# Kernel tuning notes

Measured on AMD Instinct MI355X. Metric: run time of the kernel, lower is better.

Reference implementation:

```python
import jax, jax.numpy as jnp
import numpy as np

B, HIST = 1024, 50
USER_NUM, ITEM_NUM, IN_CH = 100000, 100000, 64

def setup_inputs() -> dict:
    key = jax.random.key(0)
    k1, k2, k3, k4 = jax.random.split(key, 4)
    # xavier_uniform bound = sqrt(6/(fan_in+fan_out))
    bu = np.sqrt(6.0 / (USER_NUM + IN_CH))
    bi = np.sqrt(6.0 / (ITEM_NUM + IN_CH))
    return {
        "user_emb": jax.random.uniform(k1, (USER_NUM, IN_CH), jnp.float32, -bu, bu),
        "item_emb": jax.random.uniform(k2, (ITEM_NUM, IN_CH), jnp.float32, -bi, bi),
        "center_uid": jax.random.randint(k3, (B,), 0, USER_NUM, jnp.int32),
        "seq": jax.random.randint(k4, (B, HIST), 0, ITEM_NUM, jnp.int32),
    }

def reference(user_emb, item_emb, center_uid, seq):
    # gather selected users: [B, C]
    sel = user_emb[center_uid]
    # dense preference scores: [B, item_num]
    pref_score = sel @ item_emb.T
    b, n_items = pref_score.shape
    # boolean positive mask built by scattering seq indices per row
    rows = jnp.arange(b)[:, None]                      # [B,1]
    mask = jnp.zeros((b, n_items), bool).at[rows, seq].set(True)
    # loss = sum (s-1)^2 over positives + sum s^2 over negatives
    loss = jnp.sum(jnp.where(mask, (pref_score - 1.0) ** 2, pref_score ** 2))
    return loss, pref_score
```

## Files before the change

### kernel.cpp

```cpp
#include <hip/hip_runtime.h>

#define M_DIM 1024
#define N_DIM 100000
#define K_DIM 64
#define HIST 50

#define BM 64
#define BN 128
#define BMP 68
#define BNP 132

#define SEL_OFF 0
#define ITEM_OFF (K_DIM * BMP)
#define LDS_FLOATS (K_DIM * BMP + K_DIM * BNP)

__global__ __launch_bounds__(256, 3) void gemm_loss_kernel(
    const float* __restrict__ user_emb, const float* __restrict__ item_emb,
    const int* __restrict__ center_uid, float* __restrict__ out)
{
    __shared__ __align__(16) float lds[LDS_FLOATS];
    __shared__ float red[4];
    const int tid = threadIdx.x;
    const int bm0 = blockIdx.x * BM;
    const int bi0 = blockIdx.y * BN;

    {
        const int k4 = tid & 15;
        const int r0 = tid >> 4;
        #pragma unroll
        for (int it = 0; it < 4; ++it) {
            const int r = r0 + 16 * it;
            const int uid = center_uid[bm0 + r];
            const float4 v = *reinterpret_cast<const float4*>(
                user_emb + (size_t)uid * K_DIM + k4 * 4);
            float* p = &lds[SEL_OFF + (k4 * 4) * BMP + r];
            p[0 * BMP] = v.x; p[1 * BMP] = v.y; p[2 * BMP] = v.z; p[3 * BMP] = v.w;
        }
    }
    {
        const int k4 = tid & 15;
        const int i0 = tid >> 4;
        #pragma unroll
        for (int it = 0; it < 8; ++it) {
            const int i = i0 + 16 * it;
            const int gi = bi0 + i;
            float4 v = make_float4(0.f, 0.f, 0.f, 0.f);
            if (gi < N_DIM)
                v = *reinterpret_cast<const float4*>(
                    item_emb + (size_t)gi * K_DIM + k4 * 4);
            float* p = &lds[ITEM_OFF + (k4 * 4) * BNP + i];
            p[0 * BNP] = v.x; p[1 * BNP] = v.y; p[2 * BNP] = v.z; p[3 * BNP] = v.w;
        }
    }
    __syncthreads();

    const int tx = tid & 31;
    const int ty = tid >> 5;

    float acc[8][4];
    #pragma unroll
    for (int r = 0; r < 8; ++r)
        #pragma unroll
        for (int c = 0; c < 4; ++c) acc[r][c] = 0.f;

    const float* aBase = &lds[SEL_OFF + ty * 8];
    const float* bBase = &lds[ITEM_OFF + tx];

    #pragma unroll 8
    for (int k = 0; k < K_DIM; ++k) {
        const float4 a01 = *reinterpret_cast<const float4*>(aBase + k * BMP);
        const float4 a23 = *reinterpret_cast<const float4*>(aBase + k * BMP + 4);
        float b[4];
        #pragma unroll
        for (int c = 0; c < 4; ++c) b[c] = bBase[k * BNP + 32 * c];
        const float a[8] = {a01.x, a01.y, a01.z, a01.w, a23.x, a23.y, a23.z, a23.w};
        #pragma unroll
        for (int r = 0; r < 8; ++r)
            #pragma unroll
            for (int c = 0; c < 4; ++c)
                acc[r][c] = fmaf(a[r], b[c], acc[r][c]);
    }

    float ss = 0.f;
    float* pref = out + 1;
    #pragma unroll
    for (int r = 0; r < 8; ++r) {
        const size_t row = (size_t)(bm0 + ty * 8 + r) * N_DIM;
        #pragma unroll
        for (int c = 0; c < 4; ++c) {
            const int col = bi0 + tx + 32 * c;
            if (col < N_DIM) {
                const float v = acc[r][c];
                pref[row + col] = v;
                ss = fmaf(v, v, ss);
            }
        }
    }
    #pragma unroll
    for (int off = 32; off > 0; off >>= 1) ss += __shfl_xor(ss, off, 64);
    if ((tid & 63) == 0) red[tid >> 6] = ss;
    __syncthreads();
    if (tid == 0)
        atomicAdd(out, red[0] + red[1] + red[2] + red[3]);
}

__global__ __launch_bounds__(64) void pos_kernel(
    const float* __restrict__ user_emb, const float* __restrict__ item_emb,
    const int* __restrict__ center_uid, const int* __restrict__ seq,
    float* __restrict__ out)
{
    const int b = blockIdx.x;
    const int lane = threadIdx.x;
    const int sv = (lane < HIST) ? seq[b * HIST + lane] : -1;
    const int uid = center_uid[b];
    const float selv = user_emb[(size_t)uid * K_DIM + lane];
    float corr = 0.f;
    for (int h = 0; h < HIST; ++h) {
        const int i = __shfl(sv, h, 64);
        const unsigned long long dup = __ballot(lane < h && sv == i);
        if (dup == 0ull) {
            float p = selv * item_emb[(size_t)i * K_DIM + lane];
            #pragma unroll
            for (int off = 32; off > 0; off >>= 1) p += __shfl_xor(p, off, 64);
            if (lane == 0) corr += 1.f - 2.f * p;
        }
    }
    if (lane == 0) atomicAdd(out, corr);
}

extern "C" void kernel_launch(void* const* d_in, const int* in_sizes, int n_in,
                              void* d_out, int out_size, void* d_ws, size_t ws_size,
                              hipStream_t stream) {
    const float* user_emb  = (const float*)d_in[0];
    const float* item_emb  = (const float*)d_in[1];
    const int*   center_uid = (const int*)d_in[2];
    const int*   seq        = (const int*)d_in[3];
    float* out = (float*)d_out;

    hipMemsetAsync(out, 0, sizeof(float), stream);
    pos_kernel<<<dim3(M_DIM), dim3(64), 0, stream>>>(
        user_emb, item_emb, center_uid, seq, out);
    dim3 grid(M_DIM / BM, (N_DIM + BN - 1) / BN);
    gemm_loss_kernel<<<grid, dim3(256), 0, stream>>>(
        user_emb, item_emb, center_uid, out);
}
```

Before: 664.5 us.

## Use split-bf16 MFMA GEMM with swizzled LDS and XCD-aware tile remap

```diff
diff --git a/kernel.cpp b/kernel.cpp
--- a/kernel.cpp
+++ b/kernel.cpp
@@ -7,98 +7,148 @@
 
 #define BM 64
 #define BN 128
-#define BMP 68
-#define BNP 132
+#define NBLK_M (M_DIM / BM)
+#define NBLK_N ((N_DIM + BN - 1) / BN)
+#define NWG (NBLK_M * NBLK_N)
+#define WG_PER_XCD (NWG / 8)
 
-#define SEL_OFF 0
-#define ITEM_OFF (K_DIM * BMP)
-#define LDS_FLOATS (K_DIM * BMP + K_DIM * BNP)
+typedef __attribute__((ext_vector_type(8))) short bfrag_t;
+typedef __attribute__((ext_vector_type(16))) float accv_t;
 
-__global__ __launch_bounds__(256, 3) void gemm_loss_kernel(
+__device__ __forceinline__ unsigned short f2bf(float f) {
+    const unsigned u = __float_as_uint(f);
+    return (unsigned short)((u + 0x7FFFu + ((u >> 16) & 1u)) >> 16);
+}
+
+__global__ __launch_bounds__(256, 4) void gemm_loss_kernel(
     const float* __restrict__ user_emb, const float* __restrict__ item_emb,
     const int* __restrict__ center_uid, float* __restrict__ out)
 {
-    __shared__ __align__(16) float lds[LDS_FLOATS];
+    __shared__ __align__(16) unsigned char ldsHi[BN * 128];
+    __shared__ __align__(16) unsigned char ldsLo[BN * 128];
     __shared__ float red[4];
+
     const int tid = threadIdx.x;
-    const int bm0 = blockIdx.x * BM;
-    const int bi0 = blockIdx.y * BN;
+
+    const int bid   = blockIdx.x;
+    const int idx   = (bid & 7) * WG_PER_XCD + (bid >> 3);
+    const int itile = idx >> 4;
+    const int mtile = idx & 15;
+    const int bm0 = mtile * BM;
+    const int bi0 = itile * BN;
 
     {
-        const int k4 = tid & 15;
-        const int r0 = tid >> 4;
+        const int r  = tid >> 1;
+        const int h  = tid & 1;
+        const int gi = bi0 + r;
+        float4 v[8];
+        if (gi < N_DIM) {
+            const float* src = item_emb + (size_t)gi * K_DIM + h * 32;
+            #pragma unroll
+            for (int s = 0; s < 8; ++s)
+                v[s] = *reinterpret_cast<const float4*>(src + s * 4);
+        } else {
+            #pragma unroll
+            for (int s = 0; s < 8; ++s) v[s] = make_float4(0.f, 0.f, 0.f, 0.f);
+        }
         #pragma unroll
-        for (int it = 0; it < 4; ++it) {
-            const int r = r0 + 16 * it;
-            const int uid = center_uid[bm0 + r];
-            const float4 v = *reinterpret_cast<const float4*>(
-                user_emb + (size_t)uid * K_DIM + k4 * 4);
-            float* p = &lds[SEL_OFF + (k4 * 4) * BMP + r];
-            p[0 * BMP] = v.x; p[1 * BMP] = v.y; p[2 * BMP] = v.z; p[3 * BMP] = v.w;
+        for (int s = 0; s < 4; ++s) {
+            const float f[8] = {v[2*s].x,   v[2*s].y,   v[2*s].z,   v[2*s].w,
+                                v[2*s+1].x, v[2*s+1].y, v[2*s+1].z, v[2*s+1].w};
+            bfrag_t hv, lv;
+            #pragma unroll
+            for (int j = 0; j < 8; ++j) {
+                const unsigned short hb = f2bf(f[j]);
+                const float hf = __uint_as_float((unsigned)hb << 16);
+                hv[j] = (short)hb;
+                lv[j] = (short)f2bf(f[j] - hf);
+            }
+            int addr = r * 128 + h * 64 + s * 16;
+            addr ^= (r & 7) << 4;
+            *reinterpret_cast<bfrag_t*>(ldsHi + addr) = hv;
+            *reinterpret_cast<bfrag_t*>(ldsLo + addr) = lv;
         }
     }
-    {
-        const int k4 = tid & 15;
-        const int i0 = tid >> 4;
-        #pragma unroll
-        for (int it = 0; it < 8; ++it) {
-            const int i = i0 + 16 * it;
-            const int gi = bi0 + i;
-            float4 v = make_float4(0.f, 0.f, 0.f, 0.f);
-            if (gi < N_DIM)
-                v = *reinterpret_cast<const float4*>(
-                    item_emb + (size_t)gi * K_DIM + k4 * 4);
-            float* p = &lds[ITEM_OFF + (k4 * 4) * BNP + i];
-            p[0 * BNP] = v.x; p[1 * BNP] = v.y; p[2 * BNP] = v.z; p[3 * BNP] = v.w;
-        }
-    }
+
+    const int lane = tid & 63;
+    const int wid  = tid >> 6;
+    const int wr   = wid >> 1;
+    const int wc   = wid & 1;
+    const int lr   = lane & 31;
+    const int lg   = lane >> 5;
+
+    const int arow = bm0 + 32 * wr + lr;
+    const int uid  = center_uid[arow];
+    const float* aptr = user_emb + (size_t)uid * K_DIM + lg * 8;
+
     __syncthreads();
 
-    const int tx = tid & 31;
-    const int ty = tid >> 5;
+    accv_t acc0, acc1;
+    #pragma unroll
+    for (int i = 0; i < 16; ++i) { acc0[i] = 0.f; acc1[i] = 0.f; }
 
-    float acc[8][4];
+    const int rr0 = 64 * wc + lr;
+    const int rr1 = rr0 + 32;
+
     #pragma unroll
-    for (int r = 0; r < 8; ++r)
+    for (int ks = 0; ks < 4; ++ks) {
+        const float4 u0 = *reinterpret_cast<const float4*>(aptr + ks * 16);
+        const float4 u1 = *reinterpret_cast<const float4*>(aptr + ks * 16 + 4);
+        const float fa[8] = {u0.x, u0.y, u0.z, u0.w, u1.x, u1.y, u1.z, u1.w};
+        bfrag_t ah, al;
         #pragma unroll
-        for (int c = 0; c < 4; ++c) acc[r][c] = 0.f;
+        for (int j = 0; j < 8; ++j) {
+            const unsigned short hb = f2bf(fa[j]);
+            const float hf = __uint_as_float((unsigned)hb << 16);
+            ah[j] = (short)hb;
+            al[j] = (short)f2bf(fa[j] - hf);
+        }
+        int b0 = rr0 * 128 + ks * 32 + (lg << 4); b0 ^= (rr0 & 7) << 4;
+        int b1 = rr1 * 128 + ks * 32 + (lg << 4); b1 ^= (rr1 & 7) << 4;
+        const bfrag_t bh0 = *reinterpret_cast<const bfrag_t*>(ldsHi + b0);
+        const bfrag_t bl0 = *reinterpret_cast<const bfrag_t*>(ldsLo + b0);
+        const bfrag_t bh1 = *reinterpret_cast<const bfrag_t*>(ldsHi + b1);
+        const bfrag_t bl1 = *reinterpret_cast<const bfrag_t*>(ldsLo + b1);
 
-    const float* aBase = &lds[SEL_OFF + ty * 8];
-    const float* bBase = &lds[ITEM_OFF + tx];
-
-    #pragma unroll 8
-    for (int k = 0; k < K_DIM; ++k) {
-        const float4 a01 = *reinterpret_cast<const float4*>(aBase + k * BMP);
-        const float4 a23 = *reinterpret_cast<const float4*>(aBase + k * BMP + 4);
-        float b[4];
-        #pragma unroll
-        for (int c = 0; c < 4; ++c) b[c] = bBase[k * BNP + 32 * c];
-        const float a[8] = {a01.x, a01.y, a01.z, a01.w, a23.x, a23.y, a23.z, a23.w};
-        #pragma unroll
-        for (int r = 0; r < 8; ++r)
-            #pragma unroll
-            for (int c = 0; c < 4; ++c)
-                acc[r][c] = fmaf(a[r], b[c], acc[r][c]);
+        acc0 = __builtin_amdgcn_mfma_f32_32x32x16_bf16(ah, bh0, acc0, 0, 0, 0);
+        acc1 = __builtin_amdgcn_mfma_f32_32x32x16_bf16(ah, bh1, acc1, 0, 0, 0);
+        acc0 = __builtin_amdgcn_mfma_f32_32x32x16_bf16(ah, bl0, acc0, 0, 0, 0);
+        acc1 = __builtin_amdgcn_mfma_f32_32x32x16_bf16(ah, bl1, acc1, 0, 0, 0);
+        acc0 = __builtin_amdgcn_mfma_f32_32x32x16_bf16(al, bh0, acc0, 0, 0, 0);
+        acc1 = __builtin_amdgcn_mfma_f32_32x32x16_bf16(al, bh1, acc1, 0, 0, 0);
     }
 
     float ss = 0.f;
     float* pref = out + 1;
-    #pragma unroll
-    for (int r = 0; r < 8; ++r) {
-        const size_t row = (size_t)(bm0 + ty * 8 + r) * N_DIM;
-        #pragma unroll
-        for (int c = 0; c < 4; ++c) {
-            const int col = bi0 + tx + 32 * c;
-            if (col < N_DIM) {
-                const float v = acc[r][c];
-                pref[row + col] = v;
-                ss = fmaf(v, v, ss);
+    const int rbase = bm0 + 32 * wr + 4 * lg;
+    {
+        const int col = bi0 + 64 * wc + lr;
+        if (col < N_DIM) {
+            #pragma unroll
+            for (int r = 0; r < 16; ++r) {
+                const int row = rbase + (r & 3) + 8 * (r >> 2);
+                const float vv = acc0[r];
+                pref[(size_t)row * N_DIM + col] = vv;
+                ss = fmaf(vv, vv, ss);
             }
         }
     }
+    {
+        const int col = bi0 + 64 * wc + 32 + lr;
+        if (col < N_DIM) {
+            #pragma unroll
+            for (int r = 0; r < 16; ++r) {
+                const int row = rbase + (r & 3) + 8 * (r >> 2);
+                const float vv = acc1[r];
+                pref[(size_t)row * N_DIM + col] = vv;
+                ss = fmaf(vv, vv, ss);
+            }
+        }
+    }
+
     #pragma unroll
     for (int off = 32; off > 0; off >>= 1) ss += __shfl_xor(ss, off, 64);
-    if ((tid & 63) == 0) red[tid >> 6] = ss;
+    if (lane == 0) red[wid] = ss;
     __syncthreads();
     if (tid == 0)
         atomicAdd(out, red[0] + red[1] + red[2] + red[3]);
@@ -131,8 +181,8 @@
 extern "C" void kernel_launch(void* const* d_in, const int* in_sizes, int n_in,
                               void* d_out, int out_size, void* d_ws, size_t ws_size,
                               hipStream_t stream) {
-    const float* user_emb  = (const float*)d_in[0];
-    const float* item_emb  = (const float*)d_in[1];
+    const float* user_emb   = (const float*)d_in[0];
+    const float* item_emb   = (const float*)d_in[1];
     const int*   center_uid = (const int*)d_in[2];
     const int*   seq        = (const int*)d_in[3];
     float* out = (float*)d_out;
@@ -140,7 +190,6 @@
     hipMemsetAsync(out, 0, sizeof(float), stream);
     pos_kernel<<<dim3(M_DIM), dim3(64), 0, stream>>>(
         user_emb, item_emb, center_uid, seq, out);
-    dim3 grid(M_DIM / BM, (N_DIM + BN - 1) / BN);
-    gemm_loss_kernel<<<grid, dim3(256), 0, stream>>>(
+    gemm_loss_kernel<<<dim3(NWG), dim3(256), 0, stream>>>(
         user_emb, item_emb, center_uid, out);
 }
```

Result: faster. 593.7 us (-10.7%).
